# Kernel optimization log

Hardware: AMD Instinct MI355X
Metric: run time of the kernel (lower is better)

Reference implementation:

```python
import jax, jax.numpy as jnp
import numpy as np

EPS = 1e-6
GROUPS = 32


def setup_inputs() -> dict:
    key = jax.random.key(0)
    ks = jax.random.split(key, 6)
    B, C, T = 4, 256, 4096
    s = 1.0 / np.sqrt(C)
    return {
        "x": jax.random.normal(ks[0], (B, C, T), dtype=jnp.float32),
        "gn_scale": jnp.ones((C,), jnp.float32),
        "gn_bias": jnp.zeros((C,), jnp.float32),
        "wq": jax.random.normal(ks[1], (C, C), jnp.float32) * s,
        "bq": jnp.zeros((C,), jnp.float32),
        "wk": jax.random.normal(ks[2], (C, C), jnp.float32) * s,
        "bk": jnp.zeros((C,), jnp.float32),
        "wv": jax.random.normal(ks[3], (C, C), jnp.float32) * s,
        "bv": jnp.zeros((C,), jnp.float32),
        "wo": jax.random.normal(ks[4], (C, C), jnp.float32) * s,
        "bo": jnp.zeros((C,), jnp.float32),
    }


def _group_norm(x, scale, bias):
    B, C, T = x.shape
    h = x.reshape(B, GROUPS, C // GROUPS, T)
    mean = h.mean(axis=(2, 3), keepdims=True)
    var = ((h - mean) ** 2).mean(axis=(2, 3), keepdims=True)
    h = (h - mean) * jax.lax.rsqrt(var + EPS)
    h = h.reshape(B, C, T)
    return h * scale[None, :, None] + bias[None, :, None]


def _conv1x1(w, b, h):
    # Conv1d kernel_size=1 == per-timestep channel matmul
    return jnp.einsum('oc,bct->bot', w, h) + b[None, :, None]


def reference(x, gn_scale, gn_bias, wq, bq, wk, bk, wv, bv, wo, bo):
    B, C, T = x.shape
    h = _group_norm(x, gn_scale, gn_bias)
    q = _conv1x1(wq, bq, h)  # [B,C,T]
    k = _conv1x1(wk, bk, h)
    v = _conv1x1(wv, bv, h)
    # w_[b,q,k] = sum_c q[b,c,q] k[b,c,k] * C**-0.5, softmax over k
    w = jnp.einsum('bcq,bck->bqk', q, k) * (C ** -0.5)
    w = jax.nn.softmax(w, axis=2)
    # torch code: h_[b, i, c] = sum_j w[b, j, i] * v_perm[b, j, c]
    h = jnp.einsum('bqk,bcq->bck', w, v)  # [B,C,T]
    h = _conv1x1(wo, bo, h)
    return x + h
```

## Files before the change

kernel.cpp:

```cpp
#include <hip/hip_runtime.h>

typedef float f32x4 __attribute__((ext_vector_type(4)));
typedef short s16x8 __attribute__((ext_vector_type(8)));

__device__ __forceinline__ unsigned short f2bf(float f) {
  unsigned int u = __float_as_uint(f);
  u += 0x7fffu + ((u >> 16) & 1u);
  return (unsigned short)(u >> 16);
}

template <typename T>
__device__ __forceinline__ void gload16(const T* g, T* l) {
  __builtin_amdgcn_global_load_lds(
      (const __attribute__((address_space(1))) void*)g,
      (__attribute__((address_space(3))) void*)l, 16, 0, 0);
}

__global__ __launch_bounds__(256) void gn_stats_k(const float* __restrict__ x,
                                                  float* __restrict__ meanv,
                                                  float* __restrict__ rstdv) {
  const int bg = blockIdx.x;
  const float4* base = (const float4*)(x + (size_t)bg * 8 * 4096);
  float s = 0.f, q = 0.f;
  for (int i = threadIdx.x; i < 8192; i += 256) {
    float4 v = base[i];
    s += v.x + v.y + v.z + v.w;
    q += v.x * v.x + v.y * v.y + v.z * v.z + v.w * v.w;
  }
  for (int o = 32; o; o >>= 1) { s += __shfl_down(s, o); q += __shfl_down(q, o); }
  __shared__ float ss[4], sq[4];
  const int wv = threadIdx.x >> 6;
  if ((threadIdx.x & 63) == 0) { ss[wv] = s; sq[wv] = q; }
  __syncthreads();
  if (threadIdx.x == 0) {
    s = ss[0] + ss[1] + ss[2] + ss[3];
    q = sq[0] + sq[1] + sq[2] + sq[3];
    float mu = s * (1.f / 32768.f);
    float var = q * (1.f / 32768.f) - mu * mu;
    meanv[bg] = mu;
    rstdv[bg] = rsqrtf(var + 1e-6f);
  }
}

__global__ __launch_bounds__(256) void gn_apply_t_k(const float* __restrict__ x,
    const float* __restrict__ gamma, const float* __restrict__ beta,
    const float* __restrict__ meanv, const float* __restrict__ rstdv,
    unsigned short* __restrict__ hT) {
  __shared__ unsigned short tile[64][72];
  const int b = blockIdx.z, c0 = blockIdx.y * 64, t0 = blockIdx.x * 64;
  const int tid = threadIdx.x;
  {
    const int tr = tid >> 4, tc = (tid & 15) * 4;
    const float* xb = x + ((size_t)b * 256 + c0) * 4096 + t0;
    for (int p2 = 0; p2 < 4; ++p2) {
      int cl = p2 * 16 + tr;
      int c = c0 + cl;
      int bg = b * 32 + (c >> 3);
      float ga = gamma[c] * rstdv[bg];
      float be = beta[c] - meanv[bg] * ga;
      float4 v = *(const float4*)(xb + (size_t)cl * 4096 + tc);
      tile[cl][tc + 0] = f2bf(v.x * ga + be);
      tile[cl][tc + 1] = f2bf(v.y * ga + be);
      tile[cl][tc + 2] = f2bf(v.z * ga + be);
      tile[cl][tc + 3] = f2bf(v.w * ga + be);
    }
  }
  __syncthreads();
  {
    const int orow = tid >> 3, oc = (tid & 7) * 8;
    unsigned short* hb = hT + ((size_t)b * 4096 + t0) * 256 + c0;
    for (int p2 = 0; p2 < 2; ++p2) {
      int tl = p2 * 32 + orow;
      s16x8 w;
#pragma unroll
      for (int j = 0; j < 8; ++j) w[j] = (short)tile[oc + j][tl];
      *(s16x8*)(hb + (size_t)tl * 256 + oc) = w;
    }
  }
}

enum { EPI_WT = 0, EPI_PB = 1, EPI_PF = 2, EPI_FIN = 3 };

template <bool AF32, int EPI>
__global__ __launch_bounds__(256) void gemm64_k(
    const void* __restrict__ Ap, long long sA, int lda,
    const unsigned short* __restrict__ Bp, long long sB, int ldb,
    void* __restrict__ Op, long long sO, int ldo,
    const float* __restrict__ bias,
    const float* __restrict__ xadd, long long sX,
    float scale, int K) {
  __shared__ s16x8 lsA[4][64];
  __shared__ s16x8 lsB[4][64];
  const int tid = threadIdx.x;
  const int m0 = blockIdx.y * 64, n0 = blockIdx.x * 64;
  const int z = blockIdx.z;
  const int lane = tid & 63, wv = tid >> 6;
  const int lrow = lane & 15, lg = lane >> 4;
  const int srow = tid >> 2, scg = tid & 3;
  const int swrow = srow ^ (scg << 1);

  f32x4 acc[4];
#pragma unroll
  for (int i = 0; i < 4; ++i) acc[i] = (f32x4){0.f, 0.f, 0.f, 0.f};

  const unsigned short* Bb = Bp + (size_t)z * sB + (size_t)(n0 + srow) * ldb + scg * 8;

  for (int k0 = 0; k0 < K; k0 += 32) {
    if (AF32) {
      const float* ap = (const float*)Ap + (size_t)z * sA + (size_t)(m0 + srow) * lda + k0 + scg * 8;
      float4 v0 = *(const float4*)ap;
      float4 v1 = *(const float4*)(ap + 4);
      s16x8 w;
      w[0] = (short)f2bf(v0.x); w[1] = (short)f2bf(v0.y);
      w[2] = (short)f2bf(v0.z); w[3] = (short)f2bf(v0.w);
      w[4] = (short)f2bf(v1.x); w[5] = (short)f2bf(v1.y);
      w[6] = (short)f2bf(v1.z); w[7] = (short)f2bf(v1.w);
      lsA[scg][swrow] = w;
    } else {
      const unsigned short* ap = (const unsigned short*)Ap + (size_t)z * sA + (size_t)(m0 + srow) * lda + k0 + scg * 8;
      lsA[scg][swrow] = *(const s16x8*)ap;
    }
    lsB[scg][swrow] = *(const s16x8*)(Bb + k0);
    __syncthreads();
    s16x8 af = lsA[lg][(wv * 16 + lrow) ^ (lg << 1)];
#pragma unroll
    for (int nt = 0; nt < 4; ++nt) {
      s16x8 bf = lsB[lg][(nt * 16 + lrow) ^ (lg << 1)];
      acc[nt] = __builtin_amdgcn_mfma_f32_16x16x32_bf16(af, bf, acc[nt], 0, 0, 0);
    }
    __syncthreads();
  }

  const int mb = m0 + wv * 16 + lg * 4;
  float bv0 = 0.f, bv1 = 0.f, bv2 = 0.f, bv3 = 0.f;
  if (EPI != EPI_PF) {
    if (bias) { bv0 = bias[mb]; bv1 = bias[mb + 1]; bv2 = bias[mb + 2]; bv3 = bias[mb + 3]; }
  }
#pragma unroll
  for (int nt = 0; nt < 4; ++nt) {
    const int n = n0 + nt * 16 + lrow;
    if (EPI == EPI_WT) {
      ushort4 pk;
      pk.x = f2bf((acc[nt][0] + bv0) * scale);
      pk.y = f2bf((acc[nt][1] + bv1) * scale);
      pk.z = f2bf((acc[nt][2] + bv2) * scale);
      pk.w = f2bf((acc[nt][3] + bv3) * scale);
      *(ushort4*)((unsigned short*)Op + (size_t)z * sO + (size_t)n * ldo + mb) = pk;
    } else if (EPI == EPI_PB) {
      unsigned short* o = (unsigned short*)Op + (size_t)z * sO;
      o[(size_t)(mb + 0) * ldo + n] = f2bf(acc[nt][0] + bv0);
      o[(size_t)(mb + 1) * ldo + n] = f2bf(acc[nt][1] + bv1);
      o[(size_t)(mb + 2) * ldo + n] = f2bf(acc[nt][2] + bv2);
      o[(size_t)(mb + 3) * ldo + n] = f2bf(acc[nt][3] + bv3);
    } else if (EPI == EPI_FIN) {
      float* o = (float*)Op + (size_t)z * sO;
      const float* xa = xadd + (size_t)z * sX;
      o[(size_t)(mb + 0) * ldo + n] = acc[nt][0] + bv0 + xa[(size_t)(mb + 0) * ldo + n];
      o[(size_t)(mb + 1) * ldo + n] = acc[nt][1] + bv1 + xa[(size_t)(mb + 1) * ldo + n];
      o[(size_t)(mb + 2) * ldo + n] = acc[nt][2] + bv2 + xa[(size_t)(mb + 2) * ldo + n];
      o[(size_t)(mb + 3) * ldo + n] = acc[nt][3] + bv3 + xa[(size_t)(mb + 3) * ldo + n];
    }
  }
}

#define KS1 4
__global__ __launch_bounds__(256) void attn_stats_k(
    const unsigned short* __restrict__ qT,
    const unsigned short* __restrict__ kT,
    float* __restrict__ pm, float* __restrict__ pl) {
  __shared__ unsigned short kbuf[2][64 * 256];
  const int tid = threadIdx.x;
  const int b = blockIdx.z;
  const int Q0 = blockIdx.x * 128;
  const int kc = blockIdx.y;
  const int lane = tid & 63, w = tid >> 6;
  const int lrow = lane & 15, lg = lane >> 4;

  const unsigned short* qb = qT + (size_t)b * (4096 * 256);
  const unsigned short* kb = kT + (size_t)b * (4096 * 256);

  s16x8 af[2][8];
#pragma unroll
  for (int mt = 0; mt < 2; ++mt)
#pragma unroll
    for (int ks = 0; ks < 8; ++ks)
      af[mt][ks] = *(const s16x8*)(qb + (size_t)(Q0 + mt * 64 + w * 16 + lrow) * 256 + ks * 32 + lg * 8);

  float st_m[8], st_l[8];
#pragma unroll
  for (int s = 0; s < 8; ++s) { st_m[s] = 0.f; st_l[s] = 0.f; }

  int cur = 0;
  {
    const unsigned short* src = kb + (size_t)(kc * 1024) * 256;
#pragma unroll
    for (int rep = 0; rep < 8; ++rep) {
      int i = rep * 256 + tid;
      int row = i >> 5, c8 = i & 31;
      int c8s = c8 ^ (row & 7);
      gload16(src + (size_t)row * 256 + c8s * 8, &kbuf[0][(i - lane) * 8]);
    }
  }
  __syncthreads();

  for (int it = 0; it < 16; ++it) {
    if (it + 1 < 16) {
      const unsigned short* src = kb + (size_t)(kc * 1024 + (it + 1) * 64) * 256;
#pragma unroll
      for (int rep = 0; rep < 8; ++rep) {
        int i = rep * 256 + tid;
        int row = i >> 5, c8 = i & 31;
        int c8s = c8 ^ (row & 7);
        gload16(src + (size_t)row * 256 + c8s * 8, &kbuf[cur ^ 1][(i - lane) * 8]);
      }
    }
    f32x4 acc[2][4];
#pragma unroll
    for (int mt = 0; mt < 2; ++mt)
#pragma unroll
      for (int nt = 0; nt < 4; ++nt) acc[mt][nt] = (f32x4){0.f, 0.f, 0.f, 0.f};
#pragma unroll
    for (int ks = 0; ks < 8; ++ks) {
#pragma unroll
      for (int nt = 0; nt < 4; ++nt) {
        int row = nt * 16 + lrow;
        int ch = (ks * 4 + lg) ^ (row & 7);
        s16x8 bf = *(const s16x8*)&kbuf[cur][row * 256 + ch * 8];
        acc[0][nt] = __builtin_amdgcn_mfma_f32_16x16x32_bf16(af[0][ks], bf, acc[0][nt], 0, 0, 0);
        acc[1][nt] = __builtin_amdgcn_mfma_f32_16x16x32_bf16(af[1][ks], bf, acc[1][nt], 0, 0, 0);
      }
    }
#pragma unroll
    for (int mt = 0; mt < 2; ++mt)
#pragma unroll
      for (int j = 0; j < 4; ++j) {
        int s = mt * 4 + j;
        float v0 = acc[mt][0][j], v1 = acc[mt][1][j], v2 = acc[mt][2][j], v3 = acc[mt][3][j];
        float mx = fmaxf(fmaxf(v0, v1), fmaxf(v2, v3));
        float mn = fmaxf(st_m[s], mx);
        st_l[s] = st_l[s] * __expf(st_m[s] - mn) +
                  __expf(v0 - mn) + __expf(v1 - mn) + __expf(v2 - mn) + __expf(v3 - mn);
        st_m[s] = mn;
      }
    __syncthreads();
    cur ^= 1;
  }
#pragma unroll
  for (int s = 0; s < 8; ++s) {
    float m = st_m[s], l = st_l[s];
#pragma unroll
    for (int o = 1; o < 16; o <<= 1) {
      float mo = __shfl_xor(m, o);
      float lo = __shfl_xor(l, o);
      float mn = fmaxf(m, mo);
      l = l * __expf(m - mn) + lo * __expf(mo - mn);
      m = mn;
    }
    st_m[s] = m; st_l[s] = l;
  }
  if (lrow == 0) {
    float* pmb = pm + ((size_t)b * KS1 + kc) * 4096;
    float* plb = pl + ((size_t)b * KS1 + kc) * 4096;
#pragma unroll
    for (int mt = 0; mt < 2; ++mt)
#pragma unroll
      for (int j = 0; j < 4; ++j) {
        int q = Q0 + mt * 64 + w * 16 + lg * 4 + j;
        pmb[q] = st_m[mt * 4 + j];
        plb[q] = st_l[mt * 4 + j];
      }
  }
}

__global__ __launch_bounds__(256) void stats_merge_k(const float* __restrict__ pm,
    const float* __restrict__ pl, float* __restrict__ ma, float* __restrict__ ra) {
  int i = blockIdx.x * 256 + threadIdx.x;
  int b = i >> 12, q = i & 4095;
  const float* pmb = pm + (size_t)b * KS1 * 4096 + q;
  const float* plb = pl + (size_t)b * KS1 * 4096 + q;
  float m = -1e30f;
#pragma unroll
  for (int c = 0; c < KS1; ++c) m = fmaxf(m, pmb[(size_t)c * 4096]);
  float l = 0.f;
#pragma unroll
  for (int c = 0; c < KS1; ++c) l += plb[(size_t)c * 4096] * __expf(pmb[(size_t)c * 4096] - m);
  ma[i] = m;
  ra[i] = 1.f / l;
}

__global__ __launch_bounds__(512) void attn_pv_k(
    const unsigned short* __restrict__ qT,
    const unsigned short* __restrict__ kT,
    const unsigned short* __restrict__ vb,
    const float* __restrict__ ma, const float* __restrict__ ra,
    unsigned short* __restrict__ aT) {
  __shared__ unsigned short qbuf[2][64 * 256];
  __shared__ unsigned short vbuf[2][256 * 64];
  __shared__ unsigned short P[64 * 72];
  const int tid = threadIdx.x;
  const int b = blockIdx.y;
  const int K0 = blockIdx.x * 64;
  const int lane = tid & 63, w = tid >> 6;
  const int lrow = lane & 15, lg = lane >> 4;
  const int kr = w >> 2, qh = w & 3;
  const int cb = w * 32;

  const unsigned short* qg = qT + (size_t)b * (4096 * 256);
  const unsigned short* kg = kT + (size_t)b * (4096 * 256);
  const unsigned short* vg = vb + (size_t)b * (4096 * 256);
  const float* mg = ma + (size_t)b * 4096;
  const float* rg = ra + (size_t)b * 4096;

  s16x8 kf[2][8];
#pragma unroll
  for (int mt = 0; mt < 2; ++mt)
#pragma unroll
    for (int ks = 0; ks < 8; ++ks)
      kf[mt][ks] = *(const s16x8*)(kg + (size_t)(K0 + kr * 32 + mt * 16 + lrow) * 256 + ks * 32 + lg * 8);

  f32x4 oacc[2][4];
#pragma unroll
  for (int mt = 0; mt < 2; ++mt)
#pragma unroll
    for (int nt = 0; nt < 4; ++nt) oacc[mt][nt] = (f32x4){0.f, 0.f, 0.f, 0.f};

  int cur = 0;
  {
#pragma unroll
    for (int rep = 0; rep < 4; ++rep) {
      int i = rep * 512 + tid;
      int row = i >> 5, c8 = i & 31, c8s = c8 ^ (row & 7);
      gload16(qg + (size_t)row * 256 + c8s * 8, &qbuf[0][(i - lane) * 8]);
    }
#pragma unroll
    for (int rep = 0; rep < 4; ++rep) {
      int i = rep * 512 + tid;
      int row = i >> 3, c8 = i & 7, c8s = c8 ^ (row & 7);
      gload16(vg + (size_t)row * 4096 + c8s * 8, &vbuf[0][(i - lane) * 8]);
    }
  }
  __syncthreads();

  for (int qi = 0; qi < 64; ++qi) {
    const int q0 = qi * 64;
    if (qi + 1 < 64) {
      const unsigned short* qs = qg + (size_t)(q0 + 64) * 256;
#pragma unroll
      for (int rep = 0; rep < 4; ++rep) {
        int i = rep * 512 + tid;
        int row = i >> 5, c8 = i & 31, c8s = c8 ^ (row & 7);
        gload16(qs + (size_t)row * 256 + c8s * 8, &qbuf[cur ^ 1][(i - lane) * 8]);
      }
#pragma unroll
      for (int rep = 0; rep < 4; ++rep) {
        int i = rep * 512 + tid;
        int row = i >> 3, c8 = i & 7, c8s = c8 ^ (row & 7);
        gload16(vg + (size_t)row * 4096 + (q0 + 64) + c8s * 8, &vbuf[cur ^ 1][(i - lane) * 8]);
      }
    }
    f32x4 sacc0 = (f32x4){0.f, 0.f, 0.f, 0.f};
    f32x4 sacc1 = (f32x4){0.f, 0.f, 0.f, 0.f};
    {
      const int qrow = qh * 16 + lrow;
#pragma unroll
      for (int ks = 0; ks < 8; ++ks) {
        int ch = (ks * 4 + lg) ^ (qrow & 7);
        s16x8 bf = *(const s16x8*)&qbuf[cur][qrow * 256 + ch * 8];
        sacc0 = __builtin_amdgcn_mfma_f32_16x16x32_bf16(kf[0][ks], bf, sacc0, 0, 0, 0);
        sacc1 = __builtin_amdgcn_mfma_f32_16x16x32_bf16(kf[1][ks], bf, sacc1, 0, 0, 0);
      }
    }
    {
      const int qgl = q0 + qh * 16 + lrow;
      const float m2 = mg[qgl], rr = rg[qgl];
#pragma unroll
      for (int j = 0; j < 4; ++j) {
        P[(kr * 32 + 0 * 16 + lg * 4 + j) * 72 + qh * 16 + lrow] = f2bf(__expf(sacc0[j] - m2) * rr);
        P[(kr * 32 + 1 * 16 + lg * 4 + j) * 72 + qh * 16 + lrow] = f2bf(__expf(sacc1[j] - m2) * rr);
      }
    }
    __syncthreads();
#pragma unroll
    for (int ks = 0; ks < 2; ++ks) {
      s16x8 avf[2];
#pragma unroll
      for (int mt = 0; mt < 2; ++mt) {
        int crow = cb + mt * 16 + lrow;
        int ch = (ks * 4 + lg) ^ (crow & 7);
        avf[mt] = *(const s16x8*)&vbuf[cur][crow * 64 + ch * 8];
      }
#pragma unroll
      for (int nt = 0; nt < 4; ++nt) {
        s16x8 pf = *(const s16x8*)&P[(nt * 16 + lrow) * 72 + ks * 32 + lg * 8];
        oacc[0][nt] = __builtin_amdgcn_mfma_f32_16x16x32_bf16(avf[0], pf, oacc[0][nt], 0, 0, 0);
        oacc[1][nt] = __builtin_amdgcn_mfma_f32_16x16x32_bf16(avf[1], pf, oacc[1][nt], 0, 0, 0);
      }
    }
    __syncthreads();
    cur ^= 1;
  }
  unsigned short* ab = aT + (size_t)b * (4096 * 256);
#pragma unroll
  for (int mt = 0; mt < 2; ++mt)
#pragma unroll
    for (int nt = 0; nt < 4; ++nt) {
      int k = K0 + nt * 16 + lrow;
      int c = cb + mt * 16 + lg * 4;
      ushort4 pk;
      pk.x = f2bf(oacc[mt][nt][0]);
      pk.y = f2bf(oacc[mt][nt][1]);
      pk.z = f2bf(oacc[mt][nt][2]);
      pk.w = f2bf(oacc[mt][nt][3]);
      *(ushort4*)(ab + (size_t)k * 256 + c) = pk;
    }
}

extern "C" void kernel_launch(void* const* d_in, const int* in_sizes, int n_in,
                              void* d_out, int out_size, void* d_ws, size_t ws_size,
                              hipStream_t stream) {
  const float* x   = (const float*)d_in[0];
  const float* gns = (const float*)d_in[1];
  const float* gnb = (const float*)d_in[2];
  const float* wq  = (const float*)d_in[3];
  const float* bq  = (const float*)d_in[4];
  const float* wk  = (const float*)d_in[5];
  const float* bk  = (const float*)d_in[6];
  const float* wvp = (const float*)d_in[7];
  const float* bv  = (const float*)d_in[8];
  const float* wo  = (const float*)d_in[9];
  const float* bo  = (const float*)d_in[10];
  float* out = (float*)d_out;

  const int B = 4, C = 256, T = 4096;
  const long long TCe = (long long)T * C;

  char* p = (char*)d_ws;
  unsigned short* hT = (unsigned short*)p; p += (size_t)B * TCe * 2;
  unsigned short* qT = (unsigned short*)p; p += (size_t)B * TCe * 2;
  unsigned short* kT = (unsigned short*)p; p += (size_t)B * TCe * 2;
  unsigned short* vb = (unsigned short*)p; p += (size_t)B * TCe * 2;
  unsigned short* aT = (unsigned short*)p; p += (size_t)B * TCe * 2;
  float* gmean = (float*)p; p += 512;
  float* grstd = (float*)p; p += 512;
  float* pm = (float*)p; p += (size_t)B * KS1 * T * 4;
  float* pl = (float*)p; p += (size_t)B * KS1 * T * 4;
  float* ma = (float*)p; p += (size_t)B * T * 4;
  float* ra = (float*)p; p += (size_t)B * T * 4;

  gn_stats_k<<<B * 32, 256, 0, stream>>>(x, gmean, grstd);
  gn_apply_t_k<<<dim3(T / 64, C / 64, B), 256, 0, stream>>>(x, gns, gnb, gmean, grstd, hT);

  gemm64_k<true, EPI_WT><<<dim3(T / 64, C / 64, B), 256, 0, stream>>>(
      wq, 0, C, hT, TCe, C, qT, TCe, C, bq, nullptr, 0, 0.0625f, C);
  gemm64_k<true, EPI_WT><<<dim3(T / 64, C / 64, B), 256, 0, stream>>>(
      wk, 0, C, hT, TCe, C, kT, TCe, C, bk, nullptr, 0, 1.0f, C);
  gemm64_k<true, EPI_PB><<<dim3(T / 64, C / 64, B), 256, 0, stream>>>(
      wvp, 0, C, hT, TCe, C, vb, TCe, T, bv, nullptr, 0, 1.0f, C);

  attn_stats_k<<<dim3(T / 128, KS1, B), 256, 0, stream>>>(qT, kT, pm, pl);
  stats_merge_k<<<B * T / 256, 256, 0, stream>>>(pm, pl, ma, ra);
  attn_pv_k<<<dim3(T / 64, B), 512, 0, stream>>>(qT, kT, vb, ma, ra, aT);

  gemm64_k<true, EPI_FIN><<<dim3(T / 64, C / 64, B), 256, 0, stream>>>(
      wo, 0, C, aT, TCe, C, out, TCe, T, bo, x, TCe, 1.0f, C);
}
```

Measured before the change: 216.5 us.

## Materialize bf16 attention scores in workspace instead of recomputing QK^T in PV pass

The stats pass now writes the bf16-rounded score matrix to a workspace buffer, tiled for the PV pass, and computes its softmax statistics from those rounded values. The PV kernel reads the stored scores instead of recomputing QK^T, which removes the second Q·K matmul and the Q streaming. The PV kernel is also re-tiled to 32-key blocks with 256 threads and a single V buffer. This trades recompute for a large HBM write and read of T×T scores per batch, with batches processed in groups sized to the available workspace.

```diff
diff --git a/kernel.cpp b/kernel.cpp
--- a/kernel.cpp
+++ b/kernel.cpp
@@ -2,6 +2,7 @@
 
 typedef float f32x4 __attribute__((ext_vector_type(4)));
 typedef short s16x8 __attribute__((ext_vector_type(8)));
+typedef unsigned int u32x4 __attribute__((ext_vector_type(4)));
 
 __device__ __forceinline__ unsigned short f2bf(float f) {
   unsigned int u = __float_as_uint(f);
@@ -79,7 +80,7 @@
   }
 }
 
-enum { EPI_WT = 0, EPI_PB = 1, EPI_PF = 2, EPI_FIN = 3 };
+enum { EPI_WT = 0, EPI_PB = 1, EPI_FIN = 3 };
 
 template <bool AF32, int EPI>
 __global__ __launch_bounds__(256) void gemm64_k(
@@ -133,9 +134,7 @@
 
   const int mb = m0 + wv * 16 + lg * 4;
   float bv0 = 0.f, bv1 = 0.f, bv2 = 0.f, bv3 = 0.f;
-  if (EPI != EPI_PF) {
-    if (bias) { bv0 = bias[mb]; bv1 = bias[mb + 1]; bv2 = bias[mb + 2]; bv3 = bias[mb + 3]; }
-  }
+  if (bias) { bv0 = bias[mb]; bv1 = bias[mb + 1]; bv2 = bias[mb + 2]; bv3 = bias[mb + 3]; }
 #pragma unroll
   for (int nt = 0; nt < 4; ++nt) {
     const int n = n0 + nt * 16 + lrow;
@@ -152,7 +151,7 @@
       o[(size_t)(mb + 1) * ldo + n] = f2bf(acc[nt][1] + bv1);
       o[(size_t)(mb + 2) * ldo + n] = f2bf(acc[nt][2] + bv2);
       o[(size_t)(mb + 3) * ldo + n] = f2bf(acc[nt][3] + bv3);
-    } else if (EPI == EPI_FIN) {
+    } else {
       float* o = (float*)Op + (size_t)z * sO;
       const float* xa = xadd + (size_t)z * sX;
       o[(size_t)(mb + 0) * ldo + n] = acc[nt][0] + bv0 + xa[(size_t)(mb + 0) * ldo + n];
@@ -164,13 +163,14 @@
 }
 
 #define KS1 4
-__global__ __launch_bounds__(256) void attn_stats_k(
+__global__ __launch_bounds__(256) void attn_stats2_k(
     const unsigned short* __restrict__ qT,
     const unsigned short* __restrict__ kT,
-    float* __restrict__ pm, float* __restrict__ pl) {
+    float* __restrict__ pm, float* __restrict__ pl,
+    unsigned short* __restrict__ ST, int b0) {
   __shared__ unsigned short kbuf[2][64 * 256];
   const int tid = threadIdx.x;
-  const int b = blockIdx.z;
+  const int z = blockIdx.z, b = b0 + z;
   const int Q0 = blockIdx.x * 128;
   const int kc = blockIdx.y;
   const int lane = tid & 63, w = tid >> 6;
@@ -230,18 +230,33 @@
         acc[1][nt] = __builtin_amdgcn_mfma_f32_16x16x32_bf16(af[1][ks], bf, acc[1][nt], 0, 0, 0);
       }
     }
-#pragma unroll
-    for (int mt = 0; mt < 2; ++mt)
+    const int kt = kc * 16 + it;
+#pragma unroll
+    for (int mt = 0; mt < 2; ++mt) {
+      float sb[4][4];
+      unsigned short* tb = ST + (((size_t)(z * 64 + kt)) * 64 + (Q0 >> 6) + mt) * 4096;
+#pragma unroll
+      for (int nt = 0; nt < 4; ++nt) {
+        ushort4 pk;
+#pragma unroll
+        for (int j = 0; j < 4; ++j) {
+          unsigned short us = f2bf(acc[mt][nt][j]);
+          ((unsigned short*)&pk)[j] = us;
+          sb[nt][j] = __uint_as_float((unsigned int)us << 16);
+        }
+        *(ushort4*)(tb + (size_t)(nt * 16 + lrow) * 64 + w * 16 + lg * 4) = pk;
+      }
 #pragma unroll
       for (int j = 0; j < 4; ++j) {
         int s = mt * 4 + j;
-        float v0 = acc[mt][0][j], v1 = acc[mt][1][j], v2 = acc[mt][2][j], v3 = acc[mt][3][j];
-        float mx = fmaxf(fmaxf(v0, v1), fmaxf(v2, v3));
+        float mx = fmaxf(fmaxf(sb[0][j], sb[1][j]), fmaxf(sb[2][j], sb[3][j]));
         float mn = fmaxf(st_m[s], mx);
         st_l[s] = st_l[s] * __expf(st_m[s] - mn) +
-                  __expf(v0 - mn) + __expf(v1 - mn) + __expf(v2 - mn) + __expf(v3 - mn);
+                  __expf(sb[0][j] - mn) + __expf(sb[1][j] - mn) +
+                  __expf(sb[2][j] - mn) + __expf(sb[3][j] - mn);
         st_m[s] = mn;
       }
+    }
     __syncthreads();
     cur ^= 1;
   }
@@ -273,9 +288,9 @@
 }
 
 __global__ __launch_bounds__(256) void stats_merge_k(const float* __restrict__ pm,
-    const float* __restrict__ pl, float* __restrict__ ma, float* __restrict__ ra) {
+    const float* __restrict__ pl, float* __restrict__ ma, float* __restrict__ ra, int b0) {
   int i = blockIdx.x * 256 + threadIdx.x;
-  int b = i >> 12, q = i & 4095;
+  int b = b0 + (i >> 12), q = i & 4095;
   const float* pmb = pm + (size_t)b * KS1 * 4096 + q;
   const float* plb = pl + (size_t)b * KS1 * 4096 + q;
   float m = -1e30f;
@@ -284,128 +299,111 @@
   float l = 0.f;
 #pragma unroll
   for (int c = 0; c < KS1; ++c) l += plb[(size_t)c * 4096] * __expf(pmb[(size_t)c * 4096] - m);
-  ma[i] = m;
-  ra[i] = 1.f / l;
-}
-
-__global__ __launch_bounds__(512) void attn_pv_k(
-    const unsigned short* __restrict__ qT,
-    const unsigned short* __restrict__ kT,
+  ma[(size_t)b * 4096 + q] = m;
+  ra[(size_t)b * 4096 + q] = 1.f / l;
+}
+
+__global__ __launch_bounds__(256) void attn_pv2_k(
+    const unsigned short* __restrict__ ST,
     const unsigned short* __restrict__ vb,
     const float* __restrict__ ma, const float* __restrict__ ra,
-    unsigned short* __restrict__ aT) {
-  __shared__ unsigned short qbuf[2][64 * 256];
-  __shared__ unsigned short vbuf[2][256 * 64];
-  __shared__ unsigned short P[64 * 72];
+    unsigned short* __restrict__ aT, int b0) {
+  __shared__ unsigned short vbuf[256 * 64];
+  __shared__ unsigned short P[32 * 72];
   const int tid = threadIdx.x;
-  const int b = blockIdx.y;
-  const int K0 = blockIdx.x * 64;
+  const int z = blockIdx.y, b = b0 + z;
+  const int kb = blockIdx.x, K0 = kb * 32;
   const int lane = tid & 63, w = tid >> 6;
   const int lrow = lane & 15, lg = lane >> 4;
-  const int kr = w >> 2, qh = w & 3;
-  const int cb = w * 32;
-
-  const unsigned short* qg = qT + (size_t)b * (4096 * 256);
-  const unsigned short* kg = kT + (size_t)b * (4096 * 256);
+  const int kk_e = tid >> 3, o_e = tid & 7;
+  const int os_e = o_e ^ (kk_e & 7);
+
   const unsigned short* vg = vb + (size_t)b * (4096 * 256);
+  const unsigned short* stg = ST + ((size_t)(z * 64 + (kb >> 1)) * 64) * 4096 + (kb & 1) * 2048;
   const float* mg = ma + (size_t)b * 4096;
   const float* rg = ra + (size_t)b * 4096;
 
-  s16x8 kf[2][8];
-#pragma unroll
-  for (int mt = 0; mt < 2; ++mt)
-#pragma unroll
-    for (int ks = 0; ks < 8; ++ks)
-      kf[mt][ks] = *(const s16x8*)(kg + (size_t)(K0 + kr * 32 + mt * 16 + lrow) * 256 + ks * 32 + lg * 8);
-
-  f32x4 oacc[2][4];
-#pragma unroll
-  for (int mt = 0; mt < 2; ++mt)
-#pragma unroll
-    for (int nt = 0; nt < 4; ++nt) oacc[mt][nt] = (f32x4){0.f, 0.f, 0.f, 0.f};
-
-  int cur = 0;
+  f32x4 oacc[4][2];
+#pragma unroll
+  for (int mt = 0; mt < 4; ++mt)
+#pragma unroll
+    for (int nt = 0; nt < 2; ++nt) oacc[mt][nt] = (f32x4){0.f, 0.f, 0.f, 0.f};
+
   {
 #pragma unroll
-    for (int rep = 0; rep < 4; ++rep) {
-      int i = rep * 512 + tid;
-      int row = i >> 5, c8 = i & 31, c8s = c8 ^ (row & 7);
-      gload16(qg + (size_t)row * 256 + c8s * 8, &qbuf[0][(i - lane) * 8]);
-    }
-#pragma unroll
-    for (int rep = 0; rep < 4; ++rep) {
-      int i = rep * 512 + tid;
+    for (int rep = 0; rep < 8; ++rep) {
+      int i = rep * 256 + tid;
       int row = i >> 3, c8 = i & 7, c8s = c8 ^ (row & 7);
-      gload16(vg + (size_t)row * 4096 + c8s * 8, &vbuf[0][(i - lane) * 8]);
-    }
-  }
-  __syncthreads();
+      gload16(vg + (size_t)row * 4096 + c8s * 8, &vbuf[(i - lane) * 8]);
+    }
+  }
+  u32x4 sv = *(const u32x4*)(stg + (size_t)tid * 8);
+  float4 m4a = *(const float4*)(mg + o_e * 8);
+  float4 m4b = *(const float4*)(mg + o_e * 8 + 4);
+  float4 r4a = *(const float4*)(rg + o_e * 8);
+  float4 r4b = *(const float4*)(rg + o_e * 8 + 4);
 
   for (int qi = 0; qi < 64; ++qi) {
-    const int q0 = qi * 64;
-    if (qi + 1 < 64) {
-      const unsigned short* qs = qg + (size_t)(q0 + 64) * 256;
-#pragma unroll
-      for (int rep = 0; rep < 4; ++rep) {
-        int i = rep * 512 + tid;
-        int row = i >> 5, c8 = i & 31, c8s = c8 ^ (row & 7);
-        gload16(qs + (size_t)row * 256 + c8s * 8, &qbuf[cur ^ 1][(i - lane) * 8]);
-      }
-#pragma unroll
-      for (int rep = 0; rep < 4; ++rep) {
-        int i = rep * 512 + tid;
+    {
+      u32x4 pk;
+      float mv[8] = {m4a.x, m4a.y, m4a.z, m4a.w, m4b.x, m4b.y, m4b.z, m4b.w};
+      float rv[8] = {r4a.x, r4a.y, r4a.z, r4a.w, r4b.x, r4b.y, r4b.z, r4b.w};
+#pragma unroll
+      for (int p = 0; p < 4; ++p) {
+        unsigned int u = sv[p];
+        float s0 = __uint_as_float(u << 16);
+        float s1 = __uint_as_float(u & 0xffff0000u);
+        float p0 = __expf(s0 - mv[p * 2 + 0]) * rv[p * 2 + 0];
+        float p1 = __expf(s1 - mv[p * 2 + 1]) * rv[p * 2 + 1];
+        pk[p] = (unsigned int)f2bf(p0) | ((unsigned int)f2bf(p1) << 16);
+      }
+      *(u32x4*)&P[kk_e * 72 + os_e * 8] = pk;
+    }
+    __syncthreads();
+#pragma unroll
+    for (int ks = 0; ks < 2; ++ks) {
+      s16x8 avf[4], pf[2];
+#pragma unroll
+      for (int mt = 0; mt < 4; ++mt) {
+        int crow = w * 64 + mt * 16 + lrow;
+        int ch = (ks * 4 + lg) ^ (crow & 7);
+        avf[mt] = *(const s16x8*)&vbuf[crow * 64 + ch * 8];
+      }
+#pragma unroll
+      for (int nt = 0; nt < 2; ++nt) {
+        int kk = nt * 16 + lrow;
+        int ch = (ks * 4 + lg) ^ (kk & 7);
+        pf[nt] = *(const s16x8*)&P[kk * 72 + ch * 8];
+      }
+#pragma unroll
+      for (int mt = 0; mt < 4; ++mt)
+#pragma unroll
+        for (int nt = 0; nt < 2; ++nt)
+          oacc[mt][nt] = __builtin_amdgcn_mfma_f32_16x16x32_bf16(avf[mt], pf[nt], oacc[mt][nt], 0, 0, 0);
+    }
+    __syncthreads();
+    if (qi < 63) {
+      const int q1 = (qi + 1) * 64;
+#pragma unroll
+      for (int rep = 0; rep < 8; ++rep) {
+        int i = rep * 256 + tid;
         int row = i >> 3, c8 = i & 7, c8s = c8 ^ (row & 7);
-        gload16(vg + (size_t)row * 4096 + (q0 + 64) + c8s * 8, &vbuf[cur ^ 1][(i - lane) * 8]);
-      }
-    }
-    f32x4 sacc0 = (f32x4){0.f, 0.f, 0.f, 0.f};
-    f32x4 sacc1 = (f32x4){0.f, 0.f, 0.f, 0.f};
-    {
-      const int qrow = qh * 16 + lrow;
-#pragma unroll
-      for (int ks = 0; ks < 8; ++ks) {
-        int ch = (ks * 4 + lg) ^ (qrow & 7);
-        s16x8 bf = *(const s16x8*)&qbuf[cur][qrow * 256 + ch * 8];
-        sacc0 = __builtin_amdgcn_mfma_f32_16x16x32_bf16(kf[0][ks], bf, sacc0, 0, 0, 0);
-        sacc1 = __builtin_amdgcn_mfma_f32_16x16x32_bf16(kf[1][ks], bf, sacc1, 0, 0, 0);
-      }
-    }
-    {
-      const int qgl = q0 + qh * 16 + lrow;
-      const float m2 = mg[qgl], rr = rg[qgl];
-#pragma unroll
-      for (int j = 0; j < 4; ++j) {
-        P[(kr * 32 + 0 * 16 + lg * 4 + j) * 72 + qh * 16 + lrow] = f2bf(__expf(sacc0[j] - m2) * rr);
-        P[(kr * 32 + 1 * 16 + lg * 4 + j) * 72 + qh * 16 + lrow] = f2bf(__expf(sacc1[j] - m2) * rr);
-      }
-    }
-    __syncthreads();
-#pragma unroll
-    for (int ks = 0; ks < 2; ++ks) {
-      s16x8 avf[2];
-#pragma unroll
-      for (int mt = 0; mt < 2; ++mt) {
-        int crow = cb + mt * 16 + lrow;
-        int ch = (ks * 4 + lg) ^ (crow & 7);
-        avf[mt] = *(const s16x8*)&vbuf[cur][crow * 64 + ch * 8];
-      }
-#pragma unroll
-      for (int nt = 0; nt < 4; ++nt) {
-        s16x8 pf = *(const s16x8*)&P[(nt * 16 + lrow) * 72 + ks * 32 + lg * 8];
-        oacc[0][nt] = __builtin_amdgcn_mfma_f32_16x16x32_bf16(avf[0], pf, oacc[0][nt], 0, 0, 0);
-        oacc[1][nt] = __builtin_amdgcn_mfma_f32_16x16x32_bf16(avf[1], pf, oacc[1][nt], 0, 0, 0);
-      }
-    }
-    __syncthreads();
-    cur ^= 1;
+        gload16(vg + (size_t)row * 4096 + q1 + c8s * 8, &vbuf[(i - lane) * 8]);
+      }
+      sv = *(const u32x4*)(stg + (size_t)(qi + 1) * 4096 + tid * 8);
+      m4a = *(const float4*)(mg + q1 + o_e * 8);
+      m4b = *(const float4*)(mg + q1 + o_e * 8 + 4);
+      r4a = *(const float4*)(rg + q1 + o_e * 8);
+      r4b = *(const float4*)(rg + q1 + o_e * 8 + 4);
+    }
   }
   unsigned short* ab = aT + (size_t)b * (4096 * 256);
 #pragma unroll
-  for (int mt = 0; mt < 2; ++mt)
-#pragma unroll
-    for (int nt = 0; nt < 4; ++nt) {
+  for (int mt = 0; mt < 4; ++mt)
+#pragma unroll
+    for (int nt = 0; nt < 2; ++nt) {
       int k = K0 + nt * 16 + lrow;
-      int c = cb + mt * 16 + lg * 4;
+      int c = w * 64 + mt * 16 + lg * 4;
       ushort4 pk;
       pk.x = f2bf(oacc[mt][nt][0]);
       pk.y = f2bf(oacc[mt][nt][1]);
@@ -446,6 +444,11 @@
   float* pl = (float*)p; p += (size_t)B * KS1 * T * 4;
   float* ma = (float*)p; p += (size_t)B * T * 4;
   float* ra = (float*)p; p += (size_t)B * T * 4;
+  unsigned short* ST = (unsigned short*)p;
+  size_t used = (size_t)((char*)ST - (char*)d_ws);
+  size_t avail = ws_size > used ? ws_size - used : 0;
+  size_t perb = (size_t)T * T * 2;
+  int G = (avail >= 4 * perb) ? 4 : (avail >= 2 * perb) ? 2 : 1;
 
   gn_stats_k<<<B * 32, 256, 0, stream>>>(x, gmean, grstd);
   gn_apply_t_k<<<dim3(T / 64, C / 64, B), 256, 0, stream>>>(x, gns, gnb, gmean, grstd, hT);
@@ -457,9 +460,11 @@
   gemm64_k<true, EPI_PB><<<dim3(T / 64, C / 64, B), 256, 0, stream>>>(
       wvp, 0, C, hT, TCe, C, vb, TCe, T, bv, nullptr, 0, 1.0f, C);
 
-  attn_stats_k<<<dim3(T / 128, KS1, B), 256, 0, stream>>>(qT, kT, pm, pl);
-  stats_merge_k<<<B * T / 256, 256, 0, stream>>>(pm, pl, ma, ra);
-  attn_pv_k<<<dim3(T / 64, B), 512, 0, stream>>>(qT, kT, vb, ma, ra, aT);
+  for (int b0 = 0; b0 < B; b0 += G) {
+    attn_stats2_k<<<dim3(T / 128, KS1, G), 256, 0, stream>>>(qT, kT, pm, pl, ST, b0);
+    stats_merge_k<<<G * T / 256, 256, 0, stream>>>(pm, pl, ma, ra, b0);
+    attn_pv2_k<<<dim3(T / 32, G), 256, 0, stream>>>(ST, vb, ma, ra, aT, b0);
+  }
 
   gemm64_k<true, EPI_FIN><<<dim3(T / 64, C / 64, B), 256, 0, stream>>>(
       wo, 0, C, aT, TCe, C, out, TCe, T, bo, x, TCe, 1.0f, C);
```

Result: slower. 233.9 us (+8.1%).
